# Optimization experiments

Hardware: AMD Instinct MI355X
Metric: run time of the kernel (lower is better)

## Reference

```python
import jax, jax.numpy as jnp
import numpy as np

E = 8          # num_experts
K = 2          # top-k experts per token
CAP_RATIO = 1.05


def setup_inputs() -> dict:
    key = jax.random.key(0)
    k0, k1, k2, k3 = jax.random.split(key, 4)
    B, S, D, H = 2, 2048, 512, 2048
    return {
        "x": jax.random.normal(k0, (B, S, D), jnp.float32),
        "gate_w": jax.random.normal(k1, (E, D), jnp.float32) * (1.0 / np.sqrt(D)),
        "fc1_w": jax.random.normal(k2, (E, D, H), jnp.float32) * (1.0 / np.sqrt(D)),
        "fc1_b": jnp.zeros((E, H), jnp.float32),
        "fc2_w": jax.random.normal(k3, (E, H, D), jnp.float32) * (1.0 / np.sqrt(H)),
        "fc2_b": jnp.zeros((E, D), jnp.float32),
    }


def reference(x, gate_w, fc1_w, fc1_b, fc2_w, fc2_b):
    B, S, D = x.shape
    xf = x.reshape(-1, D)               # [T, D]
    T = xf.shape[0]

    # ---- router (eval mode: no noise) ----
    logits = xf @ gate_w.T              # [T, E]
    gates = jax.nn.softmax(logits, axis=-1)
    top_g, top_i = jax.lax.top_k(gates, K)   # [T, K]

    # importance auxiliary loss (std unbiased=False == jnp.std default)
    imp = gates.sum(axis=0)                  # [E]
    imp_loss = (jnp.std(imp) / (imp.mean() + 1e-6)) ** 2

    # ---- capacity-limited dispatch mask ----
    # torch loops slot-major: slot 0 over all tokens in order, then slot 1.
    # position of each (slot, token) entry within its expert's queue:
    buffer_cap = round(K * T * CAP_RATIO / E)
    idx_sm = top_i.T.reshape(-1)                        # [K*T] slot-major
    oh = jax.nn.one_hot(idx_sm, E, dtype=jnp.int32)     # [K*T, E]
    pos = jnp.cumsum(oh, axis=0) - oh                   # earlier same-expert count
    pos_e = jnp.take_along_axis(pos, idx_sm[:, None], axis=1)[:, 0]
    within = (pos_e < buffer_cap).reshape(K, T).T       # [T, K] bool

    wf = within.astype(xf.dtype)
    oh_tke = jax.nn.one_hot(top_i, E, dtype=xf.dtype) * wf[..., None]  # dispatch mask [T,K,E]
    combine_te = jnp.einsum('tk,tke->te', top_g * wf, oh_tke / jnp.maximum(oh_tke, 1e-30) * oh_tke) if False else jnp.einsum('tk,tke->te', top_g * wf, jax.nn.one_hot(top_i, E, dtype=xf.dtype))

    # load-balance loss from post-capacity token counts
    tokens_per_expert = oh_tke.sum(axis=(0, 1))         # [E]
    l_load = (jnp.std(tokens_per_expert) / (tokens_per_expert.mean() + 1e-6)) ** 2
    l_aux = 0.5 * (imp_loss + l_load)

    # ---- per-expert MLP (dense compute, masked combine) ----
    h = jnp.einsum('td,edh->teh', xf, fc1_w) + fc1_b[None]      # [T, E, H]
    h = jax.nn.gelu(h, approximate=False)                       # torch nn.GELU default
    y = jnp.einsum('teh,ehd->ted', h, fc2_w) + fc2_b[None]      # [T, E, D]

    out = jnp.einsum('te,ted->td', combine_te, y).reshape(B, S, D)
    return out, l_aux, l_load
```

## Files before the change

### kernel.cpp

```cpp
#include <hip/hip_runtime.h>
#include <hip/hip_bf16.h>

#define E_    8
#define TT    4096
#define DD    512
#define HH    2048
#define CAP   1075
#define MPAD  1152
#define MT    9
#define MT2   18

typedef __bf16 bf16_t;
typedef bf16_t bf16x4 __attribute__((ext_vector_type(4)));
typedef bf16_t bf16x8 __attribute__((ext_vector_type(8)));
typedef float  f32x4  __attribute__((ext_vector_type(4)));
typedef unsigned int u32;

__device__ __forceinline__ bf16_t tobf(float f) { return (bf16_t)f; }

__device__ __forceinline__ float gelu_f(float v) {
  const float u = v * (0.7978845608028654f + 0.035677408136300125f * v * v);
  const float a = __builtin_fabsf(u);
  const float ex = __expf(2.0f * a);
  float th = 1.0f - 2.0f / (ex + 1.0f);
  th = __builtin_copysignf(th, u);
  return 0.5f * v * (1.0f + th);
}

template <int N> __device__ __forceinline__ void waitcnt_vm() {
  static_assert(N == 0 || N == 4 || N == 6, "unsupported vmcnt");
  if constexpr (N == 0) asm volatile("s_waitcnt vmcnt(0)" ::: "memory");
  else if constexpr (N == 4) asm volatile("s_waitcnt vmcnt(4)" ::: "memory");
  else if constexpr (N == 6) asm volatile("s_waitcnt vmcnt(6)" ::: "memory");
}
__device__ __forceinline__ void block_barrier() {
  asm volatile("" ::: "memory");
  __builtin_amdgcn_s_barrier();
  asm volatile("" ::: "memory");
}

#define OFF_ETOK  256u
#define OFF_TOPI  (OFF_ETOK + 8u*1152u*4u)
#define OFF_TOPG  (OFF_TOPI + 4096u*2u*4u)
#define OFF_SLOT  (OFF_TOPG + 4096u*2u*4u)
#define OFF_XB    (OFF_SLOT + 4096u*2u*4u)
#define XB_BYTES  (4096u*512u*2u)
#define OFF_W1T   (OFF_XB + XB_BYTES)
#define W1T_BYTES (8u*512u*2048u*2u)
#define OFF_W2T   (OFF_W1T + W1T_BYTES)
#define W2T_BYTES (8u*2048u*512u*2u)
#define OFF_H     (OFF_W2T + W2T_BYTES)
#define H_BYTES   (8u*1152u*2048u*2u)
#define OFF_Y     OFF_W1T

__global__ __launch_bounds__(256) void prep_kernel(
    const float* __restrict__ fc1, bf16_t* __restrict__ w1t,
    const float* __restrict__ fc2, bf16_t* __restrict__ w2t,
    const float* __restrict__ x, const float* __restrict__ gw,
    float* __restrict__ imp, int* __restrict__ top_i, float* __restrict__ top_g,
    bf16_t* __restrict__ xb) {
  __shared__ float tile[64][65];
  __shared__ float simp[4][E_];
  const int bid = blockIdx.x;
  const int tid = threadIdx.x;

  if (bid < 4096) {
    const int z = bid >> 8;
    const int rem = bid & 255;
    const bool first = (z < 8);
    const int e = first ? z : z - 8;
    const int R = first ? DD : HH;
    const int C = first ? HH : DD;
    const int ct = first ? (rem & 31) : (rem & 7);
    const int rt = first ? (rem >> 5) : (rem >> 3);
    const float* ip = (first ? fc1 : fc2) + (size_t)e * DD * HH;
    bf16_t* op = (first ? w1t : w2t) + (size_t)e * DD * HH;
    const int r0 = rt * 64, c0 = ct * 64;
    const int rr = tid >> 4, c4 = (tid & 15) * 4;
#pragma unroll
    for (int p = 0; p < 4; ++p) {
      const int r = p * 16 + rr;
      const float4 v = *(const float4*)(ip + (size_t)(r0 + r) * C + c0 + c4);
      tile[r][c4 + 0] = v.x; tile[r][c4 + 1] = v.y;
      tile[r][c4 + 2] = v.z; tile[r][c4 + 3] = v.w;
    }
    __syncthreads();
    const int g = tid & 7, ob = tid >> 3;
#pragma unroll
    for (int p = 0; p < 2; ++p) {
      const int oc = p * 32 + ob;
      bf16_t o8[8];
#pragma unroll
      for (int k = 0; k < 8; ++k) o8[k] = tobf(tile[g * 8 + k][oc]);
      *(bf16x8*)(op + (size_t)(c0 + oc) * R + r0 + g * 8) = *(const bf16x8*)o8;
    }
    return;
  }

  const int rb = bid - 4096;
  const int wid = tid >> 6, lane = tid & 63;
  const int t = rb * 4 + wid;

  float p[E_];
#pragma unroll
  for (int e = 0; e < E_; ++e) p[e] = 0.f;
  const float* xr = x + (size_t)t * DD;
  bf16_t* xo = xb + (size_t)t * DD;
#pragma unroll
  for (int it = 0; it < 2; ++it) {
    const int d = it * 256 + lane * 4;
    const float4 xv = *(const float4*)(xr + d);
    bf16_t o4[4] = {tobf(xv.x), tobf(xv.y), tobf(xv.z), tobf(xv.w)};
    *(bf16x4*)(xo + d) = *(const bf16x4*)o4;
#pragma unroll
    for (int e = 0; e < E_; ++e) {
      const float4 gv = *(const float4*)(gw + e * DD + d);
      p[e] += xv.x * gv.x + xv.y * gv.y + xv.z * gv.z + xv.w * gv.w;
    }
  }
#pragma unroll
  for (int off = 32; off > 0; off >>= 1) {
#pragma unroll
    for (int e = 0; e < E_; ++e) p[e] += __shfl_down(p[e], off);
  }

  if (lane == 0) {
    float mx = p[0];
#pragma unroll
    for (int e = 1; e < E_; ++e) mx = fmaxf(mx, p[e]);
    float g[E_]; float s = 0.f;
#pragma unroll
    for (int e = 0; e < E_; ++e) { g[e] = expf(p[e] - mx); s += g[e]; }
    const float inv = 1.f / s;
#pragma unroll
    for (int e = 0; e < E_; ++e) { g[e] *= inv; simp[wid][e] = g[e]; }
    int i0 = 0;
#pragma unroll
    for (int e = 1; e < E_; ++e) if (g[e] > g[i0]) i0 = e;
    int i1 = (i0 == 0) ? 1 : 0;
#pragma unroll
    for (int e = 0; e < E_; ++e) if (e != i0 && g[e] > g[i1]) i1 = e;
    top_i[t * 2 + 0] = i0;  top_i[t * 2 + 1] = i1;
    top_g[t * 2 + 0] = g[i0]; top_g[t * 2 + 1] = g[i1];
  }
  __syncthreads();
  if (tid < E_) {
    const float s = simp[0][tid] + simp[1][tid] + simp[2][tid] + simp[3][tid];
    atomicAdd(&imp[tid], s);
  }
}

__global__ __launch_bounds__(1024) void capacity_kernel(
    const int* __restrict__ top_i, const float* __restrict__ top_g,
    const float* __restrict__ imp, int* __restrict__ etok,
    int* __restrict__ slot_map, int* __restrict__ kept, float* __restrict__ scal) {
  __shared__ u32 wt[16][4];
  const int tid = threadIdx.x, wave = tid >> 6, lane = tid & 63;

  int eidx[8];
#pragma unroll
  for (int q = 0; q < 8; ++q) {
    const int j = tid * 8 + q;
    const int k = j >> 12, t = j & (TT - 1);
    eidx[q] = top_i[t * 2 + k];
  }
  u32 pk[4] = {0u, 0u, 0u, 0u};
#pragma unroll
  for (int q = 0; q < 8; ++q) pk[eidx[q] >> 1] += 1u << ((eidx[q] & 1) * 16);

  u32 v[4] = {pk[0], pk[1], pk[2], pk[3]};
#pragma unroll
  for (int off = 1; off < 64; off <<= 1) {
#pragma unroll
    for (int p = 0; p < 4; ++p) {
      const u32 n = (u32)__shfl_up((int)v[p], off);
      if (lane >= off) v[p] += n;
    }
  }
  if (lane == 63) {
#pragma unroll
    for (int p = 0; p < 4; ++p) wt[wave][p] = v[p];
  }
  __syncthreads();
  u32 base[4] = {0u, 0u, 0u, 0u}, tot[4] = {0u, 0u, 0u, 0u};
#pragma unroll
  for (int w = 0; w < 16; ++w) {
#pragma unroll
    for (int p = 0; p < 4; ++p) {
      const u32 xv = wt[w][p];
      if (w < wave) base[p] += xv;
      tot[p] += xv;
    }
  }
  int run[E_];
#pragma unroll
  for (int p = 0; p < 4; ++p) {
    const u32 excl = base[p] + v[p] - pk[p];
    run[2 * p]     = (int)(excl & 0xFFFFu);
    run[2 * p + 1] = (int)(excl >> 16);
  }
#pragma unroll
  for (int q = 0; q < 8; ++q) {
    const int e = eidx[q];
    const int pos = run[e]++;
    const int j = tid * 8 + q;
    if (pos < CAP) {
      const int k = j >> 12, t = j & (TT - 1);
      etok[e * MPAD + pos] = t;
      slot_map[j] = (e << 16) | pos;
    } else {
      slot_map[j] = -1;
    }
  }
  if (tid == 0) {
    float tpe[E_];
#pragma unroll
    for (int p = 0; p < 4; ++p) {
      const int t0 = (int)(tot[p] & 0xFFFFu), t1 = (int)(tot[p] >> 16);
      const int k0 = t0 < CAP ? t0 : CAP, k1 = t1 < CAP ? t1 : CAP;
      kept[2 * p] = k0; kept[2 * p + 1] = k1;
      tpe[2 * p] = (float)k0; tpe[2 * p + 1] = (float)k1;
    }
    float ms = 0.f;
#pragma unroll
    for (int e = 0; e < E_; ++e) ms += tpe[e];
    ms *= (1.f / E_);
    float vt = 0.f;
#pragma unroll
    for (int e = 0; e < E_; ++e) { const float d = tpe[e] - ms; vt += d * d; }
    vt *= (1.f / E_);
    const float ll = vt / ((ms + 1e-6f) * (ms + 1e-6f));

    float iv[E_], mi = 0.f;
#pragma unroll
    for (int e = 0; e < E_; ++e) { iv[e] = imp[e]; mi += iv[e]; }
    mi *= (1.f / E_);
    float vi = 0.f;
#pragma unroll
    for (int e = 0; e < E_; ++e) { const float d = iv[e] - mi; vi += d * d; }
    vi *= (1.f / E_);
    const float il = vi / ((mi + 1e-6f) * (mi + 1e-6f));

    scal[0] = 0.5f * (il + ll);
    scal[1] = ll;
  }
}

template <int NW, int MR, int NC, int MI, int KLEN, int KSTR, bool GATHER>
__device__ __forceinline__ void gemm_core(
    const bf16_t* __restrict__ Abase, const int* __restrict__ rows,
    const bf16_t* __restrict__ B,
    bf16_t* As, bf16_t* Bs, f32x4 (&acc)[4][MI]) {
  constexpr int NWC = NC / 64;
  constexpr int AIW = MR / (8 * NW);
  constexpr int BIW = NC / (8 * NW);
  constexpr int L   = AIW + BIW;
  constexpr int NS  = KLEN / 64;
  constexpr int ABUF = MR * 64;
  constexpr int BBUF = NC * 64;
  static_assert(NS >= 2, "need >=2 K-steps");
  const int tid = threadIdx.x;
  const int wave = tid >> 6, lane = tid & 63;
  const int r8 = lane >> 3;
  const int kswz = ((lane & 7) ^ r8) * 8;
  const bf16_t* ga[AIW];
#pragma unroll
  for (int p = 0; p < AIW; ++p) {
    const int r = (wave * AIW + p) * 8 + r8;
    const int trow = GATHER ? rows[r] : r;
    ga[p] = Abase + (size_t)trow * KSTR + kswz;
  }
  const bf16_t* gb = B + (size_t)(wave * BIW * 8 + r8) * KSTR + kswz;
  const int mw = (wave / NWC) * (MI * 16), nw = (wave % NWC) * 64;
  const int l15 = lane & 15, quad = lane >> 4;
  const int sw = l15 & 7;

  auto stage = [&](int s) {
    const int k0 = s * 64;
    bf16_t* as = As + (s & 1) * ABUF;
    bf16_t* bs = Bs + (s & 1) * BBUF;
#pragma unroll
    for (int p = 0; p < AIW; ++p)
      __builtin_amdgcn_global_load_lds(
          (const __attribute__((address_space(1))) void*)(ga[p] + k0),
          (__attribute__((address_space(3))) void*)(as + ((wave * AIW + p) * 8) * 64),
          16, 0, 0);
#pragma unroll
    for (int p = 0; p < BIW; ++p)
      __builtin_amdgcn_global_load_lds(
          (const __attribute__((address_space(1))) void*)(gb + (size_t)p * 8 * KSTR + k0),
          (__attribute__((address_space(3))) void*)(bs + ((wave * BIW + p) * 8) * 64),
          16, 0, 0);
  };
  auto compute = [&](int s) {
    const bf16_t* as = As + (s & 1) * ABUF;
    const bf16_t* bs = Bs + (s & 1) * BBUF;
#pragma unroll
    for (int kh = 0; kh < 2; ++kh) {
      const int kc = ((kh * 4 + quad) ^ sw) << 3;
      bf16x8 af[MI], bfr[4];
#pragma unroll
      for (int i = 0; i < MI; ++i)
        af[i] = *(const bf16x8*)(as + (mw + i * 16 + l15) * 64 + kc);
#pragma unroll
      for (int j = 0; j < 4; ++j)
        bfr[j] = *(const bf16x8*)(bs + (nw + j * 16 + l15) * 64 + kc);
#pragma unroll
      for (int j = 0; j < 4; ++j)
#pragma unroll
        for (int i = 0; i < MI; ++i)
          acc[j][i] = __builtin_amdgcn_mfma_f32_16x16x32_bf16(bfr[j], af[i], acc[j][i], 0, 0, 0);
    }
  };

  stage(0);
  stage(1);
  waitcnt_vm<L>();
  block_barrier();

#pragma unroll
  for (int s = 0; s < NS; ++s) {
    compute(s);
    block_barrier();
    if (s + 2 < NS) {
      stage(s + 2);
      waitcnt_vm<L>();
      block_barrier();
    } else if (s + 1 < NS) {
      waitcnt_vm<0>();
      block_barrier();
    }
  }
}

__global__ __launch_bounds__(512, 4) void gemm1_kernel(
    const bf16_t* __restrict__ xb, const int* __restrict__ etok,
    const int* __restrict__ kept, const bf16_t* __restrict__ W1t,
    const float* __restrict__ b1, bf16_t* __restrict__ Hbuf) {
  const int e = blockIdx.x, tileN = blockIdx.y, tileM = blockIdx.z;
  if (tileM * 128 >= kept[e]) return;
  __shared__ __align__(16) bf16_t As[2 * 128 * 64];
  __shared__ __align__(16) bf16_t Bs[2 * 128 * 64];
  const bf16_t* B = W1t + ((size_t)e * HH + tileN * 128) * DD;
  f32x4 acc[4][2];
  const f32x4 z = {0.f, 0.f, 0.f, 0.f};
#pragma unroll
  for (int j = 0; j < 4; ++j)
#pragma unroll
    for (int i = 0; i < 2; ++i) acc[j][i] = z;
  gemm_core<8, 128, 128, 2, DD, DD, true>(xb, etok + e * MPAD + tileM * 128, B, As, Bs, acc);

  const int tid = threadIdx.x, wave = tid >> 6, lane = tid & 63;
  const int mw = (wave >> 1) * 32, nw = (wave & 1) * 64;
  const int l15 = lane & 15, quad = lane >> 4;
#pragma unroll
  for (int j = 0; j < 4; ++j) {
    const int n0 = tileN * 128 + nw + j * 16 + quad * 4;
    const float4 b4 = *(const float4*)(b1 + e * HH + n0);
#pragma unroll
    for (int i = 0; i < 2; ++i) {
      const int m = tileM * 128 + mw + i * 16 + l15;
      bf16x4 h4;
      h4.x = tobf(gelu_f(acc[j][i][0] + b4.x));
      h4.y = tobf(gelu_f(acc[j][i][1] + b4.y));
      h4.z = tobf(gelu_f(acc[j][i][2] + b4.z));
      h4.w = tobf(gelu_f(acc[j][i][3] + b4.w));
      *(bf16x4*)(Hbuf + ((size_t)e * MPAD + m) * HH + n0) = h4;
    }
  }
}

__global__ __launch_bounds__(256, 4) void gemm2_kernel(
    const bf16_t* __restrict__ Hbuf, const bf16_t* __restrict__ W2t,
    const int* __restrict__ kept, bf16_t* __restrict__ Ybuf) {
  const int e = blockIdx.x, tileN = blockIdx.y, tileM = blockIdx.z;
  const int nk = kept[e];
  if (tileM * 64 >= nk) return;
  __shared__ __align__(16) bf16_t As[2 * 64 * 64];
  __shared__ __align__(16) bf16_t Bs[2 * 128 * 64];
  const bf16_t* A = Hbuf + ((size_t)e * MPAD + tileM * 64) * HH;
  const bf16_t* B = W2t + ((size_t)e * DD + tileN * 128) * HH;
  f32x4 acc[4][2];
  const f32x4 z = {0.f, 0.f, 0.f, 0.f};
#pragma unroll
  for (int j = 0; j < 4; ++j)
#pragma unroll
    for (int i = 0; i < 2; ++i) acc[j][i] = z;
  gemm_core<4, 64, 128, 2, HH, HH, false>(A, nullptr, B, As, Bs, acc);

  const int tid = threadIdx.x, wave = tid >> 6, lane = tid & 63;
  const int mw = (wave >> 1) * 32, nw = (wave & 1) * 64;
  const int l15 = lane & 15, quad = lane >> 4;
#pragma unroll
  for (int j = 0; j < 4; ++j) {
    const int n0 = tileN * 128 + nw + j * 16 + quad * 4;
#pragma unroll
    for (int i = 0; i < 2; ++i) {
      const int m = tileM * 64 + mw + i * 16 + l15;
      if (m < nk) {
        bf16x4 o4;
        o4.x = tobf(acc[j][i][0]);
        o4.y = tobf(acc[j][i][1]);
        o4.z = tobf(acc[j][i][2]);
        o4.w = tobf(acc[j][i][3]);
        *(bf16x4*)(Ybuf + ((size_t)e * MPAD + m) * DD + n0) = o4;
      }
    }
  }
}

__global__ __launch_bounds__(128) void combine_kernel(
    const bf16_t* __restrict__ Ybuf, const float* __restrict__ b2,
    const int* __restrict__ slot_map, const float* __restrict__ top_g,
    float* __restrict__ out) {
  const int t = blockIdx.x;
  const int c = threadIdx.x * 4;
  float4 acc = {0.f, 0.f, 0.f, 0.f};
#pragma unroll
  for (int k = 0; k < 2; ++k) {
    const int sm = slot_map[k * TT + t];
    if (sm >= 0) {
      const int e = sm >> 16, pos = sm & 0xFFFF;
      const float w = top_g[t * 2 + k];
      const bf16x4 y4 = *(const bf16x4*)(Ybuf + ((size_t)e * MPAD + pos) * DD + c);
      const float4 bb = *(const float4*)(b2 + e * DD + c);
      acc.x += w * ((float)y4.x + bb.x);
      acc.y += w * ((float)y4.y + bb.y);
      acc.z += w * ((float)y4.z + bb.z);
      acc.w += w * ((float)y4.w + bb.w);
    }
  }
  *(float4*)(out + (size_t)t * DD + c) = acc;
}

extern "C" void kernel_launch(void* const* d_in, const int* in_sizes, int n_in,
                              void* d_out, int out_size, void* d_ws, size_t ws_size,
                              hipStream_t stream) {
  const float* x      = (const float*)d_in[0];
  const float* gate_w = (const float*)d_in[1];
  const float* fc1_w  = (const float*)d_in[2];
  const float* fc1_b  = (const float*)d_in[3];
  const float* fc2_w  = (const float*)d_in[4];
  const float* fc2_b  = (const float*)d_in[5];
  float* out = (float*)d_out;

  char* ws = (char*)d_ws;
  float*  imp   = (float*)(ws + 0);
  int*    kept  = (int*)(ws + 64);
  int*    etok  = (int*)(ws + OFF_ETOK);
  int*    top_i = (int*)(ws + OFF_TOPI);
  float*  top_g = (float*)(ws + OFF_TOPG);
  int*    slotm = (int*)(ws + OFF_SLOT);
  bf16_t* xb    = (bf16_t*)(ws + OFF_XB);
  bf16_t* W1t   = (bf16_t*)(ws + OFF_W1T);
  bf16_t* W2t   = (bf16_t*)(ws + OFF_W2T);
  bf16_t* Hbuf  = (bf16_t*)(ws + OFF_H);
  bf16_t* Ybuf  = (bf16_t*)(ws + OFF_Y);
  float*  scal  = out + (size_t)TT * DD;

  hipMemsetAsync(ws, 0, OFF_TOPI, stream);

  prep_kernel<<<5120, 256, 0, stream>>>(fc1_w, W1t, fc2_w, W2t,
                                        x, gate_w, imp, top_i, top_g, xb);
  capacity_kernel<<<1, 1024, 0, stream>>>(top_i, top_g, imp, etok, slotm, kept, scal);

  gemm1_kernel<<<dim3(E_, HH / 128, MT), 512, 0, stream>>>(xb, etok, kept, W1t, fc1_b, Hbuf);
  gemm2_kernel<<<dim3(E_, DD / 128, MT2), 256, 0, stream>>>(Hbuf, W2t, kept, Ybuf);
  combine_kernel<<<TT, 128, 0, stream>>>(Ybuf, fc2_b, slotm, top_g, out);
}
```

Before: 211.8 us.

## Fuse combine into gemm2 epilogue via weighted atomic scatter-add

```diff
diff --git a/kernel.cpp b/kernel.cpp
--- a/kernel.cpp
+++ b/kernel.cpp
@@ -40,7 +40,8 @@
 }
 
 #define OFF_ETOK  256u
-#define OFF_TOPI  (OFF_ETOK + 8u*1152u*4u)
+#define OFF_EWT   (OFF_ETOK + 8u*1152u*4u)
+#define OFF_TOPI  (OFF_EWT + 8u*1152u*4u)
 #define OFF_TOPG  (OFF_TOPI + 4096u*2u*4u)
 #define OFF_SLOT  (OFF_TOPG + 4096u*2u*4u)
 #define OFF_XB    (OFF_SLOT + 4096u*2u*4u)
@@ -51,7 +52,6 @@
 #define W2T_BYTES (8u*2048u*512u*2u)
 #define OFF_H     (OFF_W2T + W2T_BYTES)
 #define H_BYTES   (8u*1152u*2048u*2u)
-#define OFF_Y     OFF_W1T
 
 __global__ __launch_bounds__(256) void prep_kernel(
     const float* __restrict__ fc1, bf16_t* __restrict__ w1t,
@@ -152,8 +152,8 @@
 
 __global__ __launch_bounds__(1024) void capacity_kernel(
     const int* __restrict__ top_i, const float* __restrict__ top_g,
-    const float* __restrict__ imp, int* __restrict__ etok,
-    int* __restrict__ slot_map, int* __restrict__ kept, float* __restrict__ scal) {
+    const float* __restrict__ imp, int* __restrict__ etok, float* __restrict__ ewt,
+    int* __restrict__ kept, float* __restrict__ scal) {
   __shared__ u32 wt[16][4];
   const int tid = threadIdx.x, wave = tid >> 6, lane = tid & 63;
 
@@ -207,9 +207,7 @@
     if (pos < CAP) {
       const int k = j >> 12, t = j & (TT - 1);
       etok[e * MPAD + pos] = t;
-      slot_map[j] = (e << 16) | pos;
-    } else {
-      slot_map[j] = -1;
+      ewt[e * MPAD + pos] = top_g[t * 2 + k];
     }
   }
   if (tid == 0) {
@@ -372,7 +370,9 @@
 
 __global__ __launch_bounds__(256, 4) void gemm2_kernel(
     const bf16_t* __restrict__ Hbuf, const bf16_t* __restrict__ W2t,
-    const int* __restrict__ kept, bf16_t* __restrict__ Ybuf) {
+    const int* __restrict__ kept, const int* __restrict__ etok,
+    const float* __restrict__ ewt, const float* __restrict__ b2,
+    float* __restrict__ out) {
   const int e = blockIdx.x, tileN = blockIdx.y, tileM = blockIdx.z;
   const int nk = kept[e];
   if (tileM * 64 >= nk) return;
@@ -391,46 +391,31 @@
   const int tid = threadIdx.x, wave = tid >> 6, lane = tid & 63;
   const int mw = (wave >> 1) * 32, nw = (wave & 1) * 64;
   const int l15 = lane & 15, quad = lane >> 4;
+  int   trow[2];
+  float wgt[2];
+#pragma unroll
+  for (int i = 0; i < 2; ++i) {
+    const int m = tileM * 64 + mw + i * 16 + l15;
+    const bool live = (m < nk);
+    trow[i] = live ? etok[e * MPAD + m] : -1;
+    wgt[i]  = live ? ewt[e * MPAD + m] : 0.f;
+  }
 #pragma unroll
   for (int j = 0; j < 4; ++j) {
     const int n0 = tileN * 128 + nw + j * 16 + quad * 4;
+    const float4 b4 = *(const float4*)(b2 + e * DD + n0);
 #pragma unroll
     for (int i = 0; i < 2; ++i) {
-      const int m = tileM * 64 + mw + i * 16 + l15;
-      if (m < nk) {
-        bf16x4 o4;
-        o4.x = tobf(acc[j][i][0]);
-        o4.y = tobf(acc[j][i][1]);
-        o4.z = tobf(acc[j][i][2]);
-        o4.w = tobf(acc[j][i][3]);
-        *(bf16x4*)(Ybuf + ((size_t)e * MPAD + m) * DD + n0) = o4;
+      if (trow[i] >= 0) {
+        float* op = out + (size_t)trow[i] * DD + n0;
+        const float w = wgt[i];
+        atomicAdd(op + 0, w * (acc[j][i][0] + b4.x));
+        atomicAdd(op + 1, w * (acc[j][i][1] + b4.y));
+        atomicAdd(op + 2, w * (acc[j][i][2] + b4.z));
+        atomicAdd(op + 3, w * (acc[j][i][3] + b4.w));
       }
     }
   }
-}
-
-__global__ __launch_bounds__(128) void combine_kernel(
-    const bf16_t* __restrict__ Ybuf, const float* __restrict__ b2,
-    const int* __restrict__ slot_map, const float* __restrict__ top_g,
-    float* __restrict__ out) {
-  const int t = blockIdx.x;
-  const int c = threadIdx.x * 4;
-  float4 acc = {0.f, 0.f, 0.f, 0.f};
-#pragma unroll
-  for (int k = 0; k < 2; ++k) {
-    const int sm = slot_map[k * TT + t];
-    if (sm >= 0) {
-      const int e = sm >> 16, pos = sm & 0xFFFF;
-      const float w = top_g[t * 2 + k];
-      const bf16x4 y4 = *(const bf16x4*)(Ybuf + ((size_t)e * MPAD + pos) * DD + c);
-      const float4 bb = *(const float4*)(b2 + e * DD + c);
-      acc.x += w * ((float)y4.x + bb.x);
-      acc.y += w * ((float)y4.y + bb.y);
-      acc.z += w * ((float)y4.z + bb.z);
-      acc.w += w * ((float)y4.w + bb.w);
-    }
-  }
-  *(float4*)(out + (size_t)t * DD + c) = acc;
 }
 
 extern "C" void kernel_launch(void* const* d_in, const int* in_sizes, int n_in,
@@ -448,23 +433,22 @@
   float*  imp   = (float*)(ws + 0);
   int*    kept  = (int*)(ws + 64);
   int*    etok  = (int*)(ws + OFF_ETOK);
+  float*  ewt   = (float*)(ws + OFF_EWT);
   int*    top_i = (int*)(ws + OFF_TOPI);
   float*  top_g = (float*)(ws + OFF_TOPG);
-  int*    slotm = (int*)(ws + OFF_SLOT);
   bf16_t* xb    = (bf16_t*)(ws + OFF_XB);
   bf16_t* W1t   = (bf16_t*)(ws + OFF_W1T);
   bf16_t* W2t   = (bf16_t*)(ws + OFF_W2T);
   bf16_t* Hbuf  = (bf16_t*)(ws + OFF_H);
-  bf16_t* Ybuf  = (bf16_t*)(ws + OFF_Y);
   float*  scal  = out + (size_t)TT * DD;
 
-  hipMemsetAsync(ws, 0, OFF_TOPI, stream);
+  hipMemsetAsync(ws, 0, OFF_EWT, stream);
+  hipMemsetAsync(out, 0, (size_t)TT * DD * 4, stream);
 
   prep_kernel<<<5120, 256, 0, stream>>>(fc1_w, W1t, fc2_w, W2t,
                                         x, gate_w, imp, top_i, top_g, xb);
-  capacity_kernel<<<1, 1024, 0, stream>>>(top_i, top_g, imp, etok, slotm, kept, scal);
+  capacity_kernel<<<1, 1024, 0, stream>>>(top_i, top_g, imp, etok, ewt, kept, scal);
 
   gemm1_kernel<<<dim3(E_, HH / 128, MT), 512, 0, stream>>>(xb, etok, kept, W1t, fc1_b, Hbuf);
-  gemm2_kernel<<<dim3(E_, DD / 128, MT2), 256, 0, stream>>>(Hbuf, W2t, kept, Ybuf);
-  combine_kernel<<<TT, 128, 0, stream>>>(Ybuf, fc2_b, slotm, top_g, out);
-}
+  gemm2_kernel<<<dim3(E_, DD / 128, MT2), 256, 0, stream>>>(Hbuf, W2t, kept, etok, ewt, fc2_b, out);
+}
```

Measured after the change: 257.7 us. 21.7% more time.
